# Performance work log

Hardware: AMD Instinct MI355X
Metric: run time of the kernel (lower is better)

## Reference

```python
import jax, jax.numpy as jnp
import numpy as np

H = 512      # hidden_size == embedding_dim (required by the module's MHA)
V = 8000     # vocab_size
NH = 8       # num_heads
HD = H // NH # head_dim


def setup_inputs() -> dict:
    key = jax.random.key(0)
    ks = jax.random.split(key, 16)
    B, S, SRC = 64, 128, 256
    sc = 0.02
    return {
        "encoded_features": jax.random.normal(ks[0], (B, SRC, H), jnp.float32),
        "prev_chars": jax.random.randint(ks[1], (B, S), 0, V),
        "hidden0": jnp.zeros((B, H), jnp.float32),
        # learned params
        "embedding": jax.random.normal(ks[2], (V, H), jnp.float32) * sc,
        "in_proj_w": jax.random.normal(ks[3], (3 * H, H), jnp.float32) * sc,  # MHA packed q,k,v
        "in_proj_b": jnp.zeros((3 * H,), jnp.float32),
        "out_proj_w": jax.random.normal(ks[4], (H, H), jnp.float32) * sc,
        "out_proj_b": jnp.zeros((H,), jnp.float32),
        "gru_w_ih": jax.random.normal(ks[5], (3 * H, H + H), jnp.float32) * sc,  # input = [emb; attn]
        "gru_w_hh": jax.random.normal(ks[6], (3 * H, H), jnp.float32) * sc,
        "gru_b_ih": jnp.zeros((3 * H,), jnp.float32),
        "gru_b_hh": jnp.zeros((3 * H,), jnp.float32),
        "proj_w": jax.random.normal(ks[7], (V, H), jnp.float32) * sc,
        "proj_b": jnp.zeros((V,), jnp.float32),
    }


def _mha(q_in, kv, in_proj_w, in_proj_b, out_proj_w, out_proj_b):
    # torch nn.MultiheadAttention, batch_first=True, self q / cross kv
    wq, wk, wv = jnp.split(in_proj_w, 3, axis=0)
    bq, bk, bv = jnp.split(in_proj_b, 3, axis=0)
    B, S, _ = q_in.shape
    L = kv.shape[1]
    q = (q_in @ wq.T + bq).reshape(B, S, NH, HD)
    k = (kv @ wk.T + bk).reshape(B, L, NH, HD)
    v = (kv @ wv.T + bv).reshape(B, L, NH, HD)
    scores = jnp.einsum("bshd,blhd->bhsl", q, k) / np.sqrt(HD).astype(np.float32)
    attn = jax.nn.softmax(scores, axis=-1)
    ctx = jnp.einsum("bhsl,blhd->bshd", attn, v).reshape(B, S, H)
    return ctx @ out_proj_w.T + out_proj_b


def _gru_scan(gru_input, h0, w_ih, w_hh, b_ih, b_hh):
    # gru_input: [B, S, 2H]; torch GRUCell math, scanned over time
    def step(h, x_t):
        gi = x_t @ w_ih.T + b_ih
        gh = h @ w_hh.T + b_hh
        i_r, i_z, i_n = jnp.split(gi, 3, axis=-1)
        h_r, h_z, h_n = jnp.split(gh, 3, axis=-1)
        r = jax.nn.sigmoid(i_r + h_r)
        z = jax.nn.sigmoid(i_z + h_z)
        n = jnp.tanh(i_n + r * h_n)
        h_new = (1.0 - z) * n + z * h
        return h_new, h_new

    _, hs = jax.lax.scan(step, h0, jnp.swapaxes(gru_input, 0, 1))  # [S,B,H]
    return jnp.swapaxes(hs, 0, 1)  # [B,S,H]


def reference(encoded_features, prev_chars, hidden0, embedding, in_proj_w, in_proj_b,
              out_proj_w, out_proj_b, gru_w_ih, gru_w_hh, gru_b_ih, gru_b_hh, proj_w, proj_b):
    B, S = prev_chars.shape
    char_emb = embedding[prev_chars]                      # [B,S,H]
    query_input = char_emb + hidden0[:, None, :]          # dims match (H == E)
    attn_out = _mha(query_input, encoded_features, in_proj_w, in_proj_b, out_proj_w, out_proj_b)
    gru_input = jnp.concatenate([char_emb, attn_out], axis=-1)  # [B,S,2H]
    hidden_states = _gru_scan(gru_input, hidden0, gru_w_ih, gru_w_hh, gru_b_ih, gru_b_hh)
    logits = hidden_states @ proj_w.T + proj_b            # dropout is identity in eval
    probs = jax.nn.softmax(logits, axis=-1)
    return probs, hidden_states
```

## Files before the change

### kernel.cpp

```cpp
#include <hip/hip_runtime.h>
#include <hip/hip_bf16.h>

#define BB 64
#define SS 128
#define LSRC 256
#define HH 512
#define NHEAD 8
#define HDIM 64
#define VV 8000
#define M1 (BB*SS)
#define M2 (BB*LSRC)

typedef unsigned short u16;
typedef __attribute__((ext_vector_type(8))) short bf16x8;
typedef __attribute__((ext_vector_type(4))) float f32x4;

__device__ __forceinline__ float b2f(u16 u){
    unsigned int x = ((unsigned int)u) << 16;
    return __uint_as_float(x);
}
__device__ __forceinline__ u16 f2b(float f){
    unsigned int x = __float_as_uint(f);
    x = x + 0x7fffu + ((x >> 16) & 1u);
    return (u16)(x >> 16);
}

__global__ __launch_bounds__(256) void k_probe(const u16* __restrict__ emb, int* __restrict__ flag,
                                               int* __restrict__ bar){
    __shared__ int tot;
    if (threadIdx.x == 0) tot = 0;
    #pragma unroll
    for (int i = 0; i < 5; i++) bar[threadIdx.x + i*256] = 0;
    __syncthreads();
    int cnt = 0;
    #pragma unroll
    for (int i = 0; i < 32; i++){
        u16 u = emb[threadIdx.x * 32 + i];
        cnt += (((u >> 7) & 0xFF) >= 0x80);
    }
    #pragma unroll
    for (int off = 1; off < 64; off <<= 1) cnt += __shfl_xor(cnt, off);
    if ((threadIdx.x & 63) == 0) atomicAdd(&tot, cnt);
    __syncthreads();
    if (threadIdx.x == 0) *flag = (tot > 100) ? 1 : 0;
}

__global__ __launch_bounds__(256) void k_convert(const void* __restrict__ src, u16* __restrict__ dst,
                                                 const int* __restrict__ flag, long n8){
    long i = (long)blockIdx.x * 256 + threadIdx.x;
    if (i >= n8) return;
    if (*flag){
        const float4* s = (const float4*)src;
        float4 a = s[i*2], b = s[i*2+1];
        u16 o[8] = { f2b(a.x), f2b(a.y), f2b(a.z), f2b(a.w), f2b(b.x), f2b(b.y), f2b(b.z), f2b(b.w) };
        *(uint4*)(dst + i*8) = *(const uint4*)o;
    } else {
        *(uint4*)(dst + i*8) = ((const uint4*)src)[i];
    }
}

__global__ __launch_bounds__(256) void k_embed(const int* __restrict__ pc,
    const u16* __restrict__ emb, const u16* __restrict__ h0,
    u16* __restrict__ gruin, u16* __restrict__ qin)
{
    int c = blockIdx.x * 256 + threadIdx.x;
    int row = c >> 6;
    int kc = (c & 63) << 3;
    int b = row >> 7;
    int tok = pc[row];
    uint4 e = *(const uint4*)(emb + (long)tok * HH + kc);
    *(uint4*)(gruin + (long)row * (2*HH) + kc) = e;
    uint4 hv = *(const uint4*)(h0 + b * HH + kc);
    const u16* ep = (const u16*)&e;
    const u16* hp = (const u16*)&hv;
    u16 q[8];
    #pragma unroll
    for (int j = 0; j < 8; j++) q[j] = f2b(b2f(ep[j]) + b2f(hp[j]));
    *(uint4*)(qin + (long)row * HH + kc) = *(const uint4*)q;
}

__global__ __launch_bounds__(256) void gemm_bt(
    const u16* __restrict__ A, int lda,
    const u16* __restrict__ W, int ldw,
    const u16* __restrict__ bias,
    u16* __restrict__ Cb, float* __restrict__ Cf, int ldc,
    int N, int K)
{
    __shared__ u16 As[128*64];
    __shared__ u16 Bs[128*64];
    const int tid = threadIdx.x;
    const int wave = tid >> 6, lane = tid & 63;
    const int m0 = blockIdx.x * 128, n0 = blockIdx.y * 128;
    const int wm = (wave & 1) * 64, wn = (wave >> 1) * 64;
    const int lm = lane & 15, lq = lane >> 4;
    f32x4 acc[4][4];
    #pragma unroll
    for (int i = 0; i < 4; i++)
        #pragma unroll
        for (int j = 0; j < 4; j++) acc[i][j] = (f32x4){0.f,0.f,0.f,0.f};

    for (int k0 = 0; k0 < K; k0 += 64) {
        #pragma unroll
        for (int i = 0; i < 4; i++) {
            int chunk = i*256 + tid;
            int row = chunk >> 3, kc = (chunk & 7) << 3;
            *(uint4*)(As + chunk*8) = *(const uint4*)(A + (long)(m0+row)*lda + k0 + kc);
            int brow = n0 + row; if (brow >= N) brow = N - 1;
            *(uint4*)(Bs + chunk*8) = *(const uint4*)(W + (long)brow*ldw + k0 + kc);
        }
        __syncthreads();
        #pragma unroll
        for (int kk = 0; kk < 64; kk += 32) {
            bf16x8 af[4], bfr[4];
            #pragma unroll
            for (int i = 0; i < 4; i++){
                af[i]  = *(const bf16x8*)(As + (wm + i*16 + lm)*64 + kk + lq*8);
                bfr[i] = *(const bf16x8*)(Bs + (wn + i*16 + lm)*64 + kk + lq*8);
            }
            #pragma unroll
            for (int mi = 0; mi < 4; mi++)
                #pragma unroll
                for (int ni = 0; ni < 4; ni++)
                    acc[mi][ni] = __builtin_amdgcn_mfma_f32_16x16x32_bf16(af[mi], bfr[ni], acc[mi][ni], 0, 0, 0);
        }
        __syncthreads();
    }
    #pragma unroll
    for (int ni = 0; ni < 4; ni++){
        int n = n0 + wn + ni*16 + lm;
        if (n >= N) continue;
        float bv = bias ? b2f(bias[n]) : 0.f;
        #pragma unroll
        for (int mi = 0; mi < 4; mi++){
            #pragma unroll
            for (int r = 0; r < 4; r++){
                int m = m0 + wm + mi*16 + lq*4 + r;
                float v = acc[mi][ni][r] + bv;
                if (Cf) Cf[(long)m*ldc + n] = v;
                else    Cb[(long)m*ldc + n] = f2b(v);
            }
        }
    }
}

__global__ __launch_bounds__(256) void k_attn(const u16* __restrict__ Qb,
    const u16* __restrict__ Kb, const u16* __restrict__ Vb, u16* __restrict__ ctxb)
{
    __shared__ u16 smem[64*264 + 4*32*264];
    u16* Vt = smem;
    u16* Ks = smem + 64*264;
    u16* Ps = smem + 64*264;
    const int bid = blockIdx.x;
    const int h = bid & 7, b = bid >> 3;
    const int tid = threadIdx.x;
    const int wave = tid >> 6, lane = tid & 63;
    const int lm = lane & 15, lq = lane >> 4;
    const long kvbase = (long)b*LSRC*HH + h*HDIM;

    #pragma unroll
    for (int i = 0; i < 8; i++){
        int c = i*256 + tid;
        int l = c >> 3, ch0 = (c & 7) << 3;
        uint4 kv = *(const uint4*)(Kb + kvbase + (long)l*HH + ch0);
        *(uint4*)(Ks + l*72 + ch0) = kv;
        uint4 vv = *(const uint4*)(Vb + kvbase + (long)l*HH + ch0);
        const u16* vp = (const u16*)&vv;
        #pragma unroll
        for (int j = 0; j < 8; j++) Vt[(ch0 + j)*264 + l] = vp[j];
    }

    bf16x8 aq[2][2];
    #pragma unroll
    for (int mt = 0; mt < 2; mt++)
        #pragma unroll
        for (int kk = 0; kk < 2; kk++)
            aq[mt][kk] = *(const bf16x8*)(Qb + (long)(b*SS + wave*32 + mt*16 + lm)*HH
                                              + h*HDIM + kk*32 + lq*8);
    __syncthreads();

    f32x4 accs[2][16];
    #pragma unroll
    for (int mt = 0; mt < 2; mt++)
        #pragma unroll
        for (int nt = 0; nt < 16; nt++) accs[mt][nt] = (f32x4){0.f,0.f,0.f,0.f};
    #pragma unroll
    for (int nt = 0; nt < 16; nt++){
        bf16x8 bk0 = *(const bf16x8*)(Ks + (nt*16 + lm)*72 +  0 + lq*8);
        bf16x8 bk1 = *(const bf16x8*)(Ks + (nt*16 + lm)*72 + 32 + lq*8);
        #pragma unroll
        for (int mt = 0; mt < 2; mt++){
            accs[mt][nt] = __builtin_amdgcn_mfma_f32_16x16x32_bf16(aq[mt][0], bk0, accs[mt][nt], 0, 0, 0);
            accs[mt][nt] = __builtin_amdgcn_mfma_f32_16x16x32_bf16(aq[mt][1], bk1, accs[mt][nt], 0, 0, 0);
        }
    }

    float mxv[2][4];
    #pragma unroll
    for (int mt = 0; mt < 2; mt++)
        #pragma unroll
        for (int r = 0; r < 4; r++){
            float m = -1e30f;
            #pragma unroll
            for (int nt = 0; nt < 16; nt++) m = fmaxf(m, accs[mt][nt][r]);
            m *= 0.125f;
            m = fmaxf(m, __shfl_xor(m, 1));
            m = fmaxf(m, __shfl_xor(m, 2));
            m = fmaxf(m, __shfl_xor(m, 4));
            m = fmaxf(m, __shfl_xor(m, 8));
            mxv[mt][r] = m;
        }
    float smv[2][4] = {{0.f,0.f,0.f,0.f},{0.f,0.f,0.f,0.f}};
    #pragma unroll
    for (int mt = 0; mt < 2; mt++)
        #pragma unroll
        for (int nt = 0; nt < 16; nt++)
            #pragma unroll
            for (int r = 0; r < 4; r++){
                float p = __expf(accs[mt][nt][r]*0.125f - mxv[mt][r]);
                smv[mt][r] += p;
                accs[mt][nt][r] = p;
            }
    float inv[2][4];
    #pragma unroll
    for (int mt = 0; mt < 2; mt++)
        #pragma unroll
        for (int r = 0; r < 4; r++){
            float s = smv[mt][r];
            s += __shfl_xor(s, 1); s += __shfl_xor(s, 2);
            s += __shfl_xor(s, 4); s += __shfl_xor(s, 8);
            inv[mt][r] = 1.f / s;
        }

    __syncthreads();
    const int woff = wave * (32*264);
    #pragma unroll
    for (int mt = 0; mt < 2; mt++)
        #pragma unroll
        for (int nt = 0; nt < 16; nt++)
            #pragma unroll
            for (int r = 0; r < 4; r++)
                Ps[woff + (mt*16 + lq*4 + r)*264 + nt*16 + lm] = f2b(accs[mt][nt][r]);
    __syncthreads();

    f32x4 accc[2][4];
    #pragma unroll
    for (int mt = 0; mt < 2; mt++)
        #pragma unroll
        for (int nt = 0; nt < 4; nt++) accc[mt][nt] = (f32x4){0.f,0.f,0.f,0.f};
    #pragma unroll
    for (int kk = 0; kk < 8; kk++){
        bf16x8 pa0 = *(const bf16x8*)(Ps + woff + ( 0 + lm)*264 + kk*32 + lq*8);
        bf16x8 pa1 = *(const bf16x8*)(Ps + woff + (16 + lm)*264 + kk*32 + lq*8);
        #pragma unroll
        for (int nt = 0; nt < 4; nt++){
            bf16x8 bv = *(const bf16x8*)(Vt + (nt*16 + lm)*264 + kk*32 + lq*8);
            accc[0][nt] = __builtin_amdgcn_mfma_f32_16x16x32_bf16(pa0, bv, accc[0][nt], 0, 0, 0);
            accc[1][nt] = __builtin_amdgcn_mfma_f32_16x16x32_bf16(pa1, bv, accc[1][nt], 0, 0, 0);
        }
    }

    #pragma unroll
    for (int mt = 0; mt < 2; mt++)
        #pragma unroll
        for (int nt = 0; nt < 4; nt++)
            #pragma unroll
            for (int r = 0; r < 4; r++){
                int srow = wave*32 + mt*16 + lq*4 + r;
                int ch = nt*16 + lm;
                float v = accc[mt][nt][r] * inv[mt][r];
                ctxb[(long)(b*SS + srow)*HH + h*HDIM + ch] = f2b(v);
            }
}

__global__ __launch_bounds__(256) void k_gru_all(
    const float* __restrict__ gi, const u16* __restrict__ whh, const u16* __restrict__ bhh,
    const u16* __restrict__ h0b, u16* __restrict__ hx0, u16* __restrict__ hx1,
    u16* __restrict__ hout, int* __restrict__ bar)
{
    __shared__ u16 wlds[48*520];
    const int tid = threadIdx.x;
    const int bid = blockIdx.x;
    const int j0 = bid * 16;
    const int wave = tid >> 6, lane = tid & 63;
    const int lm = lane & 15, lq = lane >> 4;

    #pragma unroll
    for (int i = 0; i < 12; i++){
        int c = i*256 + tid;
        int rl = c >> 6, kc = (c & 63) << 3;
        int g = rl >> 4, jr = rl & 15;
        *(uint4*)(wlds + rl*520 + kc) = *(const uint4*)(whh + (long)(g*512 + j0 + jr)*HH + kc);
    }
    __syncthreads();

    const int j = j0 + lm;
    const float br = b2f(bhh[j]), bz = b2f(bhh[512 + j]), bn = b2f(bhh[1024 + j]);
    const int brow = wave*16 + lm;
    float hp[4];
    #pragma unroll
    for (int r = 0; r < 4; r++) hp[r] = b2f(h0b[(wave*16 + lq*4 + r)*HH + j]);

    const u16* hsrc = h0b;
    for (int s = 0; s < SS; s++){
        bf16x8 af[16];
        #pragma unroll
        for (int k = 0; k < 16; k++)
            af[k] = *(const bf16x8*)(hsrc + (long)brow*HH + k*32 + lq*8);
        float gir[4], giz[4], gin[4];
        #pragma unroll
        for (int r = 0; r < 4; r++){
            int b = wave*16 + lq*4 + r;
            long gbase = (long)(b*SS + s)*1536;
            gir[r] = gi[gbase + j];
            giz[r] = gi[gbase + 512 + j];
            gin[r] = gi[gbase + 1024 + j];
        }
        __builtin_amdgcn_sched_barrier(0);
        f32x4 acc[3];
        acc[0] = (f32x4){0.f,0.f,0.f,0.f};
        acc[1] = acc[0]; acc[2] = acc[0];
        #pragma unroll
        for (int k = 0; k < 16; k++){
            #pragma unroll
            for (int g = 0; g < 3; g++){
                bf16x8 wf = *(const bf16x8*)(wlds + (g*16 + lm)*520 + k*32 + lq*8);
                acc[g] = __builtin_amdgcn_mfma_f32_16x16x32_bf16(af[k], wf, acc[g], 0, 0, 0);
            }
        }
        u16* hdst = (s & 1) ? hx1 : hx0;
        #pragma unroll
        for (int r = 0; r < 4; r++){
            int b = wave*16 + lq*4 + r;
            float rg = 1.f/(1.f + __expf(-(gir[r] + acc[0][r] + br)));
            float zg = 1.f/(1.f + __expf(-(giz[r] + acc[1][r] + bz)));
            float ng = tanhf(gin[r] + rg*(acc[2][r] + bn));
            float hv = (1.f - zg)*ng + zg*hp[r];
            hp[r] = hv;
            u16 hb = f2b(hv);
            hdst[b*HH + j] = hb;
            hout[(long)(b*SS + s)*HH + j] = hb;
        }
        __syncthreads();
        if (tid == 0){
            __threadfence();
            __hip_atomic_store(&bar[bid*32], s+1, __ATOMIC_RELAXED, __HIP_MEMORY_SCOPE_AGENT);
        }
        if (tid < 32){
            while (__hip_atomic_load(&bar[tid*32], __ATOMIC_RELAXED, __HIP_MEMORY_SCOPE_AGENT) <= s)
                __builtin_amdgcn_s_sleep(1);
        }
        __syncthreads();
        __threadfence();
        hsrc = hdst;
    }
}

__global__ __launch_bounds__(256) void k_softmax(const u16* __restrict__ logits, void* __restrict__ out,
                                                 const int* __restrict__ flag)
{
    __shared__ float red[4];
    __shared__ float red2[4];
    long row = blockIdx.x;
    const u16* p = logits + row*VV;
    int tid = threadIdx.x, wave = tid >> 6, lane = tid & 63;
    float v[32];
    float mx = -1e30f;
    #pragma unroll
    for (int i = 0; i < 32; i++){
        int c = tid + i*256;
        v[i] = (c < VV) ? b2f(p[c]) : -1e30f;
        mx = fmaxf(mx, v[i]);
    }
    #pragma unroll
    for (int off = 1; off < 64; off <<= 1) mx = fmaxf(mx, __shfl_xor(mx, off));
    if (lane == 0) red[wave] = mx;
    __syncthreads();
    mx = fmaxf(fmaxf(red[0], red[1]), fmaxf(red[2], red[3]));
    float sum = 0.f;
    #pragma unroll
    for (int i = 0; i < 32; i++){
        int c = tid + i*256;
        if (c < VV){ v[i] = __expf(v[i] - mx); sum += v[i]; }
    }
    #pragma unroll
    for (int off = 1; off < 64; off <<= 1) sum += __shfl_xor(sum, off);
    if (lane == 0) red2[wave] = sum;
    __syncthreads();
    float inv = 1.f / (red2[0] + red2[1] + red2[2] + red2[3]);
    int f = *flag;
    float* pf = (float*)out + row*VV;
    u16*  pb = (u16*)out + row*VV;
    #pragma unroll
    for (int i = 0; i < 32; i++){
        int c = tid + i*256;
        if (c < VV){
            float r = v[i]*inv;
            if (f) pf[c] = r; else pb[c] = f2b(r);
        }
    }
}

__global__ __launch_bounds__(256) void k_hidout(const u16* __restrict__ hid, void* __restrict__ out,
                                                const int* __restrict__ flag)
{
    long i = (long)blockIdx.x * 256 + threadIdx.x;
    u16 h = hid[i];
    if (*flag) ((float*)out + (size_t)M1*VV)[i] = b2f(h);
    else       ((u16*)out  + (size_t)M1*VV)[i] = h;
}

extern "C" void kernel_launch(void* const* d_in, const int* in_sizes, int n_in,
                              void* d_out, int out_size, void* d_ws, size_t ws_size,
                              hipStream_t stream)
{
    const int* pc = (const int*)d_in[1];

    const size_t MB = 1u << 20;
    char* w = (char*)d_ws;
    u16* qin   = (u16*)(w + 0);
    u16* ctxb  = (u16*)(w + 0);
    u16* Qb    = (u16*)(w + 8*MB);
    u16* Kb    = (u16*)(w + 16*MB);
    u16* Vb    = (u16*)(w + 32*MB);
    u16* gruin = (u16*)(w + 48*MB);
    float* gi  = (float*)(w + 0);
    u16* logits= (u16*)(w + 0);
    u16* enc_b = (u16*)(w + 126*MB);
    u16* emb_b = (u16*)(w + 142*MB);
    u16* pw_b  = (u16*)(w + 150*MB);
    u16* wih_b = (u16*)(w + 158*MB);
    u16* whh_b = (u16*)(w + 161*MB);
    u16* ipw_b = (u16*)(w + 163*MB);
    u16* opw_b = (u16*)(w + 165*MB);
    u16* h0_b  = (u16*)(w + 166*MB);
    u16* ipb_b = (u16*)(w + 166*MB + 128*1024);
    u16* opb_b = (u16*)(w + 166*MB + 192*1024);
    u16* bih_b = (u16*)(w + 166*MB + 256*1024);
    u16* bhh_b = (u16*)(w + 166*MB + 320*1024);
    u16* pb_b  = (u16*)(w + 166*MB + 384*1024);
    int* flag  = (int*)(w + 166*MB + 448*1024);
    int* bar   = (int*)(w + 166*MB + 452*1024);
    u16* hx0   = (u16*)(w + 167*MB);
    u16* hx1   = (u16*)(w + 167*MB + 128*1024);
    u16* hid_b = (u16*)(w + 168*MB);

    k_probe<<<1, 256, 0, stream>>>((const u16*)d_in[3], flag, bar);
    struct { const void* s; u16* d; long n; } cv[13] = {
        { d_in[0],  enc_b, (long)M2*HH },
        { d_in[2],  h0_b,  BB*HH },
        { d_in[3],  emb_b, (long)VV*HH },
        { d_in[4],  ipw_b, 3*HH*HH },
        { d_in[5],  ipb_b, 3*HH },
        { d_in[6],  opw_b, HH*HH },
        { d_in[7],  opb_b, HH },
        { d_in[8],  wih_b, 3L*HH*2*HH },
        { d_in[9],  whh_b, 3*HH*HH },
        { d_in[10], bih_b, 3*HH },
        { d_in[11], bhh_b, 3*HH },
        { d_in[12], pw_b,  (long)VV*HH },
        { d_in[13], pb_b,  VV },
    };
    for (int i = 0; i < 13; i++){
        long n8 = cv[i].n >> 3;
        k_convert<<<(int)((n8 + 255)/256), 256, 0, stream>>>(cv[i].s, cv[i].d, flag, n8);
    }

    k_embed<<<2048, 256, 0, stream>>>(pc, emb_b, h0_b, gruin, qin);
    gemm_bt<<<dim3(64,4),  256, 0, stream>>>(qin,   HH, ipw_b,            HH, ipb_b,      Qb,  nullptr, HH,  HH, HH);
    gemm_bt<<<dim3(128,4), 256, 0, stream>>>(enc_b, HH, ipw_b + 512*512,  HH, ipb_b+512,  Kb,  nullptr, HH,  HH, HH);
    gemm_bt<<<dim3(128,4), 256, 0, stream>>>(enc_b, HH, ipw_b + 1024*512, HH, ipb_b+1024, Vb,  nullptr, HH,  HH, HH);
    k_attn<<<BB*NHEAD, 256, 0, stream>>>(Qb, Kb, Vb, ctxb);
    gemm_bt<<<dim3(64,4),  256, 0, stream>>>(ctxb, HH, opw_b, HH, opb_b, gruin + 512, nullptr, 2*HH, HH, HH);
    gemm_bt<<<dim3(64,12), 256, 0, stream>>>(gruin, 2*HH, wih_b, 2*HH, bih_b, nullptr, gi, 1536, 1536, 2*HH);

    {
        const float* gia = gi; const u16* whha = whh_b; const u16* bhha = bhh_b;
        const u16* h0a = h0_b; u16* hx0a = hx0; u16* hx1a = hx1; u16* hida = hid_b;
        int* bara = bar;
        void* gru_args[] = { (void*)&gia, (void*)&whha, (void*)&bhha, (void*)&h0a,
                             (void*)&hx0a, (void*)&hx1a, (void*)&hida, (void*)&bara };
        hipLaunchCooperativeKernel((const void*)k_gru_all, dim3(32), dim3(256),
                                   gru_args, 0, stream);
    }

    gemm_bt<<<dim3(64,63), 256, 0, stream>>>(hid_b, HH, pw_b, HH, pb_b, logits, nullptr, VV, VV, HH);
    k_softmax<<<M1, 256, 0, stream>>>(logits, d_out, flag);
    k_hidout<<<16384, 256, 0, stream>>>(hid_b, d_out, flag);
}
```

Measured before the change: 1.569 ms.

## Restructure GRU step barrier: drop fences, pack h stores, prefetch next gi

The recurrent GRU kernel's per-step grid barrier now relies on relaxed agent-scope atomic loads and stores of the hidden state instead of __threadfence calls. Lanes exchange neighbouring bf16 values with a shuffle and write them as packed 32-bit stores. The hout write-back and the next step's gi loads move in after the barrier signal so they overlap with the spin-wait. The intent is a shorter serialized per-step critical path across 128 steps. The risk is memory ordering: visibility now depends on relaxed atomics with no fence before the flag store.

```diff
diff --git a/kernel.cpp b/kernel.cpp
--- a/kernel.cpp
+++ b/kernel.cpp
@@ -300,20 +300,25 @@
     #pragma unroll
     for (int r = 0; r < 4; r++) hp[r] = b2f(h0b[(wave*16 + lq*4 + r)*HH + j]);
 
+    float gir[4], giz[4], gin[4];
+    #pragma unroll
+    for (int r = 0; r < 4; r++){
+        int b = wave*16 + lq*4 + r;
+        long gbase = (long)(b*SS + 0)*1536;
+        gir[r] = gi[gbase + j];
+        giz[r] = gi[gbase + 512 + j];
+        gin[r] = gi[gbase + 1024 + j];
+    }
+
     const u16* hsrc = h0b;
     for (int s = 0; s < SS; s++){
-        bf16x8 af[16];
-        #pragma unroll
-        for (int k = 0; k < 16; k++)
-            af[k] = *(const bf16x8*)(hsrc + (long)brow*HH + k*32 + lq*8);
-        float gir[4], giz[4], gin[4];
-        #pragma unroll
-        for (int r = 0; r < 4; r++){
-            int b = wave*16 + lq*4 + r;
-            long gbase = (long)(b*SS + s)*1536;
-            gir[r] = gi[gbase + j];
-            giz[r] = gi[gbase + 512 + j];
-            gin[r] = gi[gbase + 1024 + j];
+        union { unsigned u[4]; bf16x8 v; } af[16];
+        #pragma unroll
+        for (int k = 0; k < 16; k++){
+            const unsigned* ab = (const unsigned*)(hsrc + (long)brow*HH + k*32 + lq*8);
+            #pragma unroll
+            for (int i = 0; i < 4; i++)
+                af[k].u[i] = __hip_atomic_load(ab + i, __ATOMIC_RELAXED, __HIP_MEMORY_SCOPE_AGENT);
         }
         __builtin_amdgcn_sched_barrier(0);
         f32x4 acc[3];
@@ -324,33 +329,68 @@
             #pragma unroll
             for (int g = 0; g < 3; g++){
                 bf16x8 wf = *(const bf16x8*)(wlds + (g*16 + lm)*520 + k*32 + lq*8);
-                acc[g] = __builtin_amdgcn_mfma_f32_16x16x32_bf16(af[k], wf, acc[g], 0, 0, 0);
+                acc[g] = __builtin_amdgcn_mfma_f32_16x16x32_bf16(af[k].v, wf, acc[g], 0, 0, 0);
             }
         }
         u16* hdst = (s & 1) ? hx1 : hx0;
+        u16 hbv[4];
         #pragma unroll
         for (int r = 0; r < 4; r++){
-            int b = wave*16 + lq*4 + r;
             float rg = 1.f/(1.f + __expf(-(gir[r] + acc[0][r] + br)));
             float zg = 1.f/(1.f + __expf(-(giz[r] + acc[1][r] + bz)));
             float ng = tanhf(gin[r] + rg*(acc[2][r] + bn));
             float hv = (1.f - zg)*ng + zg*hp[r];
             hp[r] = hv;
-            u16 hb = f2b(hv);
-            hdst[b*HH + j] = hb;
-            hout[(long)(b*SS + s)*HH + j] = hb;
-        }
-        __syncthreads();
-        if (tid == 0){
-            __threadfence();
-            __hip_atomic_store(&bar[bid*32], s+1, __ATOMIC_RELAXED, __HIP_MEMORY_SCOPE_AGENT);
-        }
-        if (tid < 32){
-            while (__hip_atomic_load(&bar[tid*32], __ATOMIC_RELAXED, __HIP_MEMORY_SCOPE_AGENT) <= s)
-                __builtin_amdgcn_s_sleep(1);
-        }
-        __syncthreads();
-        __threadfence();
+            hbv[r] = f2b(hv);
+        }
+        unsigned pk[4];
+        #pragma unroll
+        for (int r = 0; r < 4; r++){
+            unsigned nb = (unsigned)__shfl_xor((int)(unsigned)hbv[r], 1);
+            pk[r] = (unsigned)hbv[r] | (nb << 16);
+        }
+        if ((lm & 1) == 0){
+            #pragma unroll
+            for (int r = 0; r < 4; r++){
+                int b = wave*16 + lq*4 + r;
+                __hip_atomic_store((unsigned*)(hdst + b*HH + j), pk[r],
+                                   __ATOMIC_RELAXED, __HIP_MEMORY_SCOPE_AGENT);
+            }
+        }
+        if (s + 1 < SS){
+            __syncthreads();
+            if (tid == 0)
+                __hip_atomic_store(&bar[bid*32], s+1, __ATOMIC_RELAXED, __HIP_MEMORY_SCOPE_AGENT);
+            if ((lm & 1) == 0){
+                #pragma unroll
+                for (int r = 0; r < 4; r++){
+                    int b = wave*16 + lq*4 + r;
+                    *(unsigned*)(hout + (long)(b*SS + s)*HH + j) = pk[r];
+                }
+            }
+            #pragma unroll
+            for (int r = 0; r < 4; r++){
+                int b = wave*16 + lq*4 + r;
+                long gbase = (long)(b*SS + s+1)*1536;
+                gir[r] = gi[gbase + j];
+                giz[r] = gi[gbase + 512 + j];
+                gin[r] = gi[gbase + 1024 + j];
+            }
+            if (tid < 32){
+                while (__hip_atomic_load(&bar[tid*32], __ATOMIC_RELAXED, __HIP_MEMORY_SCOPE_AGENT) <= s)
+                    __builtin_amdgcn_s_sleep(1);
+            }
+            __syncthreads();
+            asm volatile("" ::: "memory");
+        } else {
+            if ((lm & 1) == 0){
+                #pragma unroll
+                for (int r = 0; r < 4; r++){
+                    int b = wave*16 + lq*4 + r;
+                    *(unsigned*)(hout + (long)(b*SS + s)*HH + j) = pk[r];
+                }
+            }
+        }
         hsrc = hdst;
     }
 }
```

Result: slower. 1.892 ms (+20.6%).
